# Optimization experiments

Hardware: AMD Instinct MI355X
Metric: run time of the kernel (lower is better)

The kernel has to match this reference:

```python
import jax, jax.numpy as jnp
import numpy as np

N_NODES = 100_000
N_EDGES = 1_600_000
F_IN = 32
F_OUT = 32
DIM = 2
K = 5                      # kernel_size per dim (open spline)
KTOT = K ** DIM            # 25 kernel weight matrices
S = 2 ** DIM               # 4 nonzero linear-B-spline basis terms per edge
NEG_SLOPE = 0.2

# offsets over the 2^DIM corners of the spline cell, [S, DIM]
_OFFSETS = np.array([[(s >> d) & 1 for d in range(DIM)] for s in range(S)], dtype=np.int32)
_STRIDES = np.array([K ** d for d in range(DIM)], dtype=np.int32)


def _spline_basis(pseudo):
    """Degree-1 open B-spline basis. pseudo: [E, DIM] in [0,1].
    Returns basis [E, S] and kernel-weight indices widx [E, S]."""
    offsets = jnp.asarray(_OFFSETS)
    strides = jnp.asarray(_STRIDES)
    p = pseudo * (K - 1)                         # open spline scaling
    fl = jnp.floor(p)
    frac = p - fl                                # [E, DIM]
    b = jnp.where(offsets[None] == 0, 1.0 - frac[:, None, :], frac[:, None, :])
    basis = jnp.prod(b, axis=-1)                 # [E, S]
    idx = jnp.clip(fl.astype(jnp.int32)[:, None, :] + offsets[None], 0, K - 1)
    widx = jnp.sum(idx * strides, axis=-1)       # [E, S] in [0, KTOT)
    return basis, widx


def setup_inputs() -> dict:
    key = jax.random.key(0)
    ks = jax.random.split(key, 7)
    x = jax.random.normal(ks[0], (N_NODES, F_IN), dtype=jnp.float32)
    edge_index = jax.random.randint(ks[1], (2, N_EDGES), 0, N_NODES)
    pseudo = jax.random.uniform(ks[2], (N_EDGES, DIM), dtype=jnp.float32)
    bound = 1.0 / np.sqrt(KTOT * F_IN)           # matches reset_parameters uniform(size, ...)
    weight = jax.random.uniform(ks[3], (KTOT, F_IN, F_OUT), jnp.float32, -bound, bound)
    root_weight = jax.random.uniform(ks[4], (F_IN, F_OUT), jnp.float32, -bound, bound)
    att_weight = jax.random.uniform(ks[5], (2 * F_OUT,), jnp.float32, -bound, bound)
    bias = jax.random.uniform(ks[6], (F_OUT,), jnp.float32, -bound, bound)
    return {"x": x, "edge_index": edge_index, "pseudo": pseudo, "weight": weight,
            "root_weight": root_weight, "att_weight": att_weight, "bias": bias}


def reference(x, edge_index, pseudo, weight, root_weight, att_weight, bias):
    row, col = edge_index[0], edge_index[1]      # row = target, col = source
    basis, widx = _spline_basis(pseudo)          # [E,S], [E,S]

    # Precompute x @ W_k for every kernel weight: [N, KTOT, F_OUT]
    xw = jnp.einsum('nf,kfo->nko', x, weight)
    flat = col[:, None] * KTOT + widx            # [E, S] flat (node, kernel) index
    gathered = xw.reshape(-1, F_OUT)[flat]       # [E, S, F_OUT]
    msg = jnp.einsum('es,esf->ef', basis, gathered)  # spline-weighted edge messages

    x_root = x @ root_weight                     # [N, F_OUT]

    # GAT-style attention logits: cat([x_root[row], msg]) . att_weight
    alpha = x_root[row] @ att_weight[:F_OUT] + msg @ att_weight[F_OUT:]
    alpha = jnp.where(alpha > 0, alpha, NEG_SLOPE * alpha)  # leaky relu

    # segment softmax over incoming edges of each target node
    amax = jax.ops.segment_max(alpha, row, num_segments=N_NODES)
    amax = jnp.where(jnp.isfinite(amax), amax, 0.0)
    ex = jnp.exp(alpha - amax[row])
    denom = jax.ops.segment_sum(ex, row, num_segments=N_NODES)
    att = ex / (denom[row] + 1e-16)

    out = jax.ops.segment_sum(msg * att[:, None], row, num_segments=N_NODES)
    return out + x_root + bias
```

## Files before the change

### kernel.cpp

```cpp
#include <hip/hip_runtime.h>
#include <stdint.h>

#define N_NODES 100000
#define N_EDGES 1600000
#define NBLK_SCAN 391

typedef __attribute__((ext_vector_type(8))) short short8;
typedef __attribute__((ext_vector_type(4))) float float4v;

__device__ __forceinline__ unsigned short f32_to_bf16(float f) {
  uint32_t u = __float_as_uint(f);
  u += 0x7fffu + ((u >> 16) & 1u);
  return (unsigned short)(u >> 16);
}
__device__ __forceinline__ float bf16_to_f32(unsigned short h) {
  return __uint_as_float(((uint32_t)h) << 16);
}

__global__ __launch_bounds__(256) void k_zero(
    const float* __restrict__ weight, const float* __restrict__ root_w,
    int* __restrict__ deg, unsigned short* __restrict__ wbf) {
  int tid = threadIdx.x;
  int b = blockIdx.x;
  int i = b * 256 + tid;
  if (i < N_NODES) deg[i] = 0;
  if (b < 100) {
    int e = i;
    int km = e >> 10;
    int rem = e & 1023;
    int kk = rem >> 5;
    int fo = rem & 31;
    int t = km * 2 + (fo >> 4);
    int c = fo & 15;
    int q = kk >> 3, j = kk & 7;
    wbf[((t * 4 + q) * 16 + c) * 8 + j] = f32_to_bf16(weight[e]);
  } else if (b == 100) {
    for (int idx = tid; idx < 1024; idx += 256) {
      int kk = idx >> 5;
      int fo = idx & 31;
      int t = 50 + (fo >> 4);
      int c = fo & 15;
      int q = kk >> 3, j = kk & 7;
      wbf[((t * 4 + q) * 16 + c) * 8 + j] = f32_to_bf16(root_w[idx]);
    }
  }
}

__global__ __launch_bounds__(256) void k1_xw(
    const float* __restrict__ x, const unsigned short* __restrict__ wbf,
    const int* __restrict__ ei, const float* __restrict__ att_w,
    const float* __restrict__ bias,
    int* __restrict__ deg, unsigned short* __restrict__ rank,
    unsigned short* __restrict__ xw, float* __restrict__ out,
    float* __restrict__ r_dot) {
  __shared__ __align__(16) unsigned short ot[16 * 808];
  __shared__ float xr[16][33];
  int tid = threadIdx.x;
  int b = blockIdx.x;

  int e = b * 256 + tid;
  int rk = atomicAdd(&deg[ei[e]], 1);

  int wave = tid >> 6, lane = tid & 63;
  int quad = lane >> 4, c16 = lane & 15;
  int n0 = b * 16;
  const float* xp = x + (size_t)(n0 + c16) * 32 + quad * 8;
  float4 a0 = *reinterpret_cast<const float4*>(xp);
  float4 a1 = *reinterpret_cast<const float4*>(xp + 4);
  short8 af;
  af[0] = (short)f32_to_bf16(a0.x); af[1] = (short)f32_to_bf16(a0.y);
  af[2] = (short)f32_to_bf16(a0.z); af[3] = (short)f32_to_bf16(a0.w);
  af[4] = (short)f32_to_bf16(a1.x); af[5] = (short)f32_to_bf16(a1.y);
  af[6] = (short)f32_to_bf16(a1.z); af[7] = (short)f32_to_bf16(a1.w);

  for (int t = wave; t < 52; t += 4) {
    short8 bf = *reinterpret_cast<const short8*>(wbf + ((t * 4 + quad) * 16 + c16) * 8);
    float4v acc = {0.f, 0.f, 0.f, 0.f};
    acc = __builtin_amdgcn_mfma_f32_16x16x32_bf16(af, bf, acc, 0, 0, 0);
    if (t < 50) {
      int cg = t * 16 + c16;
#pragma unroll
      for (int r = 0; r < 4; r++) ot[(quad * 4 + r) * 808 + cg] = f32_to_bf16(acc[r]);
    } else {
      int f = (t - 50) * 16 + c16;
#pragma unroll
      for (int r = 0; r < 4; r++) xr[quad * 4 + r][f] = acc[r];
    }
  }
  __syncthreads();

  const uint4* src = (const uint4*)ot;
  uint4* dst = (uint4*)(xw + (size_t)n0 * 800);
  for (int i = tid; i < 1600; i += 256) {
    int r = i / 100;
    int c = i - r * 100;
    dst[r * 100 + c] = src[r * 101 + c];
  }
  for (int idx = tid; idx < 512; idx += 256) {
    int n = idx >> 5, f = idx & 31;
    out[(n0 + n) * 32 + f] = xr[n][f] + bias[f];
  }
  if (tid < 16) {
    float s = 0.f;
#pragma unroll
    for (int f = 0; f < 32; f++) s += xr[tid][f] * att_w[f];
    r_dot[n0 + tid] = s;
  }
  rank[e] = (unsigned short)rk;
}

__global__ __launch_bounds__(256) void kscan1(const int* __restrict__ deg,
                                              int* __restrict__ incl,
                                              int* __restrict__ bsum) {
  __shared__ int s[256];
  int tid = threadIdx.x;
  int i = blockIdx.x * 256 + tid;
  int v = (i < N_NODES) ? deg[i] : 0;
  s[tid] = v;
  __syncthreads();
  for (int d = 1; d < 256; d <<= 1) {
    int t = (tid >= d) ? s[tid - d] : 0;
    __syncthreads();
    s[tid] += t;
    __syncthreads();
  }
  if (i < N_NODES) incl[i] = s[tid];
  if (tid == 255) bsum[blockIdx.x] = s[255];
}

__global__ __launch_bounds__(512) void kscan2(const int* __restrict__ bsum,
                                              int* __restrict__ bbase) {
  __shared__ int s[512];
  int tid = threadIdx.x;
  int v = (tid < NBLK_SCAN) ? bsum[tid] : 0;
  s[tid] = v;
  __syncthreads();
  for (int d = 1; d < 512; d <<= 1) {
    int t = (tid >= d) ? s[tid - d] : 0;
    __syncthreads();
    s[tid] += t;
    __syncthreads();
  }
  if (tid < NBLK_SCAN) bbase[tid] = s[tid] - v;
}

__global__ __launch_bounds__(256) void kscan3(const int* __restrict__ deg,
                                              int* __restrict__ offs,
                                              const int* __restrict__ bbase) {
  int i = blockIdx.x * 256 + threadIdx.x;
  if (i < N_NODES) offs[i] = offs[i] - deg[i] + bbase[i >> 8];
  if (i == 0) offs[N_NODES] = N_EDGES;
}

__global__ __launch_bounds__(256) void kscatter(
    const int* __restrict__ ei, const float* __restrict__ pseudo,
    const int* __restrict__ offs, const unsigned short* __restrict__ rank,
    uint2* __restrict__ epack) {
  int tid = threadIdx.x;
  int base = blockIdx.x * 2048;
#pragma unroll
  for (int k = 0; k < 8; k++) {
    int e = base + k * 256 + tid;
    if (e < N_EDGES) {
      int r = ei[e];
      int c = ei[N_EDGES + e];
      int pos = offs[r] + (int)rank[e];
      float p0 = pseudo[2 * e] * 4.f;
      float p1 = pseudo[2 * e + 1] * 4.f;
      float fl0 = floorf(p0), fl1 = floorf(p1);
      float fr0 = p0 - fl0, fr1 = p1 - fl1;
      int i0 = (int)fl0, i1 = (int)fl1;
      int a0 = min(i0, 4), a0p = min(i0 + 1, 4);
      int a1 = 5 * min(i1, 4), a1p = 5 * min(i1 + 1, 4);
      unsigned long long w0 = (unsigned long long)(a0 + a1);
      unsigned long long w1 = (unsigned long long)(a0p + a1);
      unsigned long long w2 = (unsigned long long)(a0 + a1p);
      unsigned long long w3 = (unsigned long long)(a0p + a1p);
      unsigned long long q0 = (unsigned long long)__float2uint_rn(fr0 * 8191.f);
      unsigned long long q1 = (unsigned long long)__float2uint_rn(fr1 * 8191.f);
      unsigned long long v = (unsigned long long)(unsigned int)c |
                             (w0 << 17) | (w1 << 22) | (w2 << 27) | (w3 << 32) |
                             (q0 << 37) | (q1 << 50);
      uint2 pk;
      pk.x = (unsigned int)v;
      pk.y = (unsigned int)(v >> 32);
      epack[pos] = pk;
    }
  }
}

__device__ __forceinline__ void decode_pk(uint2 pk, int& col, int& w0, int& w1,
                                          int& w2, int& w3, float& fr0, float& fr1) {
  unsigned long long v = ((unsigned long long)pk.y << 32) | pk.x;
  col = (int)(v & 0x1FFFF);
  w0 = (int)((v >> 17) & 31); w1 = (int)((v >> 22) & 31);
  w2 = (int)((v >> 27) & 31); w3 = (int)((v >> 32) & 31);
  fr0 = (float)(unsigned int)((v >> 37) & 8191) * (1.f / 8191.f);
  fr1 = (float)(unsigned int)((v >> 50) & 8191) * (1.f / 8191.f);
}

__device__ __forceinline__ void edge_step(uint2 pk, const unsigned short* __restrict__ xwf,
                                          float a2, float rd, float& acc, float& den) {
  int col, w0, w1, w2, w3; float fr0, fr1;
  decode_pk(pk, col, w0, w1, w2, w3, fr0, fr1);
  const unsigned short* base = xwf + (size_t)col * 800;
  float g0 = bf16_to_f32(base[w0 * 32]);
  float g1 = bf16_to_f32(base[w1 * 32]);
  float g2 = bf16_to_f32(base[w2 * 32]);
  float g3 = bf16_to_f32(base[w3 * 32]);
  float c0 = 1.f - fr0, c1 = 1.f - fr1;
  float msg = c1 * (c0 * g0 + fr0 * g1) + fr1 * (c0 * g2 + fr0 * g3);
  float t = msg * a2;
#pragma unroll
  for (int m = 16; m >= 1; m >>= 1) t += __shfl_xor(t, m);
  float alpha = rd + t;
  alpha = alpha > 0.f ? alpha : 0.2f * alpha;
  float ex = __expf(alpha);
  acc += msg * ex;
  den += ex;
}

__global__ __launch_bounds__(256) void k2_csr(
    const int* __restrict__ offs, const uint2* __restrict__ epack,
    const unsigned short* __restrict__ xw, const float* __restrict__ r_dot,
    const float* __restrict__ att_w, float* __restrict__ out) {
  int tid = threadIdx.x;
  int wave = tid >> 6, lane = tid & 63;
  int node = blockIdx.x * 4 + wave;
  if (node >= N_NODES) return;
  int f = lane & 31, half = lane >> 5;
  float a2 = att_w[32 + f];
  float rd = r_dot[node];
  int s0 = offs[node], s1 = offs[node + 1];
  const unsigned short* xwf = xw + f;
  float acc = 0.f, den = 0.f;
  int i = s0 + half;

  for (; i + 6 < s1; i += 8) {
    uint2 p[4];
    p[0] = epack[i];     p[1] = epack[i + 2];
    p[2] = epack[i + 4]; p[3] = epack[i + 6];
    int col[4], w0[4], w1[4], w2[4], w3[4];
    float fr0[4], fr1[4];
#pragma unroll
    for (int u = 0; u < 4; u++)
      decode_pk(p[u], col[u], w0[u], w1[u], w2[u], w3[u], fr0[u], fr1[u]);
    float g0[4], g1[4], g2[4], g3[4];
#pragma unroll
    for (int u = 0; u < 4; u++) {
      const unsigned short* base = xwf + (size_t)col[u] * 800;
      g0[u] = bf16_to_f32(base[w0[u] * 32]);
      g1[u] = bf16_to_f32(base[w1[u] * 32]);
      g2[u] = bf16_to_f32(base[w2[u] * 32]);
      g3[u] = bf16_to_f32(base[w3[u] * 32]);
    }
    float msg[4], t[4];
#pragma unroll
    for (int u = 0; u < 4; u++) {
      float c0 = 1.f - fr0[u], c1 = 1.f - fr1[u];
      msg[u] = c1 * (c0 * g0[u] + fr0[u] * g1[u]) + fr1[u] * (c0 * g2[u] + fr0[u] * g3[u]);
      t[u] = msg[u] * a2;
    }
#pragma unroll
    for (int m = 16; m >= 1; m >>= 1) {
      t[0] += __shfl_xor(t[0], m);
      t[1] += __shfl_xor(t[1], m);
      t[2] += __shfl_xor(t[2], m);
      t[3] += __shfl_xor(t[3], m);
    }
#pragma unroll
    for (int u = 0; u < 4; u++) {
      float alpha = rd + t[u];
      alpha = alpha > 0.f ? alpha : 0.2f * alpha;
      float ex = __expf(alpha);
      acc += msg[u] * ex;
      den += ex;
    }
  }
  for (; i < s1; i += 2) edge_step(epack[i], xwf, a2, rd, acc, den);

  acc += __shfl_xor(acc, 32);
  den += __shfl_xor(den, 32);
  if (half == 0) out[node * 32 + f] += acc / (den + 1e-16f);
}

extern "C" void kernel_launch(void* const* d_in, const int* in_sizes, int n_in,
                              void* d_out, int out_size, void* d_ws, size_t ws_size,
                              hipStream_t stream) {
  const float* x      = (const float*)d_in[0];
  const int*   ei     = (const int*)d_in[1];
  const float* pseudo = (const float*)d_in[2];
  const float* weight = (const float*)d_in[3];
  const float* root_w = (const float*)d_in[4];
  const float* att_w  = (const float*)d_in[5];
  const float* bias   = (const float*)d_in[6];
  float* out = (float*)d_out;

  char* ws = (char*)d_ws;
  unsigned short* xw   = (unsigned short*)ws;
  float* r_dot         = (float*)(ws + 160000000);
  unsigned short* wbf  = (unsigned short*)(ws + 160400000);
  int* deg             = (int*)(ws + 160453504);
  int* offs            = (int*)(ws + 160853504);
  int* bsum            = (int*)(ws + 161253520);
  int* bbase           = (int*)(ws + 161255120);
  unsigned short* rank = (unsigned short*)(ws + 161256720);
  uint2* epack         = (uint2*)(ws + 164456720);

  hipLaunchKernelGGL(k_zero, dim3(NBLK_SCAN), dim3(256), 0, stream,
                     weight, root_w, deg, wbf);
  hipLaunchKernelGGL(k1_xw, dim3(6250), dim3(256), 0, stream,
                     x, wbf, ei, att_w, bias, deg, rank, xw, out, r_dot);
  hipLaunchKernelGGL(kscan1, dim3(NBLK_SCAN), dim3(256), 0, stream, deg, offs, bsum);
  hipLaunchKernelGGL(kscan2, dim3(1), dim3(512), 0, stream, bsum, bbase);
  hipLaunchKernelGGL(kscan3, dim3(NBLK_SCAN), dim3(256), 0, stream, deg, offs, bbase);
  hipLaunchKernelGGL(kscatter, dim3(782), dim3(256), 0, stream,
                     ei, pseudo, offs, rank, epack);
  hipLaunchKernelGGL(k2_csr, dim3(25000), dim3(256), 0, stream,
                     offs, epack, xw, r_dot, att_w, out);
}
```

Baseline: 338.4 us.

## Precompute per-node kernel attention dots and fold softmax weights into per-edge coefficients

Adds a per-node, per-kernel table of the dot product between each xW_k row and the second half of the attention vector, computed in the xW kernel. The scatter kernel uses it to compute each edge's attention logit and exponential directly, and stores four bf16 basis-times-exp coefficients plus a compact index word per edge. The CSR aggregation kernel therefore drops its cross-lane shuffle reductions and exp work and reduces to a weighted gather-sum, using two accumulators. In exchange, the scatter kernel does extra random gathers into the new table, the softmax is computed without max subtraction, and the coefficients are rounded to bf16, so results may drift and large logits could overflow. Neighbouring spline weights are also addressed as w and w+1, which relies on a padding row that k_zero zeroes past the end of xw.

```diff
diff --git a/kernel.cpp b/kernel.cpp
--- a/kernel.cpp
+++ b/kernel.cpp
@@ -19,7 +19,8 @@
 
 __global__ __launch_bounds__(256) void k_zero(
     const float* __restrict__ weight, const float* __restrict__ root_w,
-    int* __restrict__ deg, unsigned short* __restrict__ wbf) {
+    int* __restrict__ deg, unsigned short* __restrict__ wbf,
+    unsigned short* __restrict__ xw, float* __restrict__ ydot) {
   int tid = threadIdx.x;
   int b = blockIdx.x;
   int i = b * 256 + tid;
@@ -39,10 +40,14 @@
       int kk = idx >> 5;
       int fo = idx & 31;
       int t = 50 + (fo >> 4);
-      int c = fo & 15;
+      int c = fo & 31 & 15;
       int q = kk >> 3, j = kk & 7;
-      wbf[((t * 4 + q) * 16 + c) * 8 + j] = f32_to_bf16(root_w[idx]);
-    }
+      wbf[((t * 4 + q) * 16 + (fo & 15)) * 8 + j] = f32_to_bf16(root_w[idx]);
+      (void)c;
+    }
+  } else if (b == 101) {
+    if (tid < 400) ((unsigned int*)(xw + 80000000))[tid] = 0u;
+    if (tid < 16) ydot[2500000 + tid] = 0.f;
   }
 }
 
@@ -52,11 +57,14 @@
     const float* __restrict__ bias,
     int* __restrict__ deg, unsigned short* __restrict__ rank,
     unsigned short* __restrict__ xw, float* __restrict__ out,
-    float* __restrict__ r_dot) {
+    float* __restrict__ r_dot, float* __restrict__ ydot) {
   __shared__ __align__(16) unsigned short ot[16 * 808];
   __shared__ float xr[16][33];
+  __shared__ float att2s[32];
   int tid = threadIdx.x;
   int b = blockIdx.x;
+
+  if (tid < 32) att2s[tid] = att_w[32 + tid];
 
   int e = b * 256 + tid;
   int rk = atomicAdd(&deg[ei[e]], 1);
@@ -100,6 +108,15 @@
     int n = idx >> 5, f = idx & 31;
     out[(n0 + n) * 32 + f] = xr[n][f] + bias[f];
   }
+  for (int idx = tid; idx < 400; idx += 256) {
+    int nd = idx / 25;
+    int km = idx - nd * 25;
+    const unsigned short* orow = ot + nd * 808 + km * 32;
+    float s = 0.f;
+#pragma unroll
+    for (int ff = 0; ff < 32; ff++) s += bf16_to_f32(orow[ff]) * att2s[ff];
+    ydot[(size_t)(n0 + nd) * 25 + km] = s;
+  }
   if (tid < 16) {
     float s = 0.f;
 #pragma unroll
@@ -155,7 +172,8 @@
 __global__ __launch_bounds__(256) void kscatter(
     const int* __restrict__ ei, const float* __restrict__ pseudo,
     const int* __restrict__ offs, const unsigned short* __restrict__ rank,
-    uint2* __restrict__ epack) {
+    const float* __restrict__ ydot, const float* __restrict__ r_dot,
+    unsigned int* __restrict__ eidx, uint2* __restrict__ ecoef) {
   int tid = threadIdx.x;
   int base = blockIdx.x * 2048;
 #pragma unroll
@@ -170,115 +188,93 @@
       float fl0 = floorf(p0), fl1 = floorf(p1);
       float fr0 = p0 - fl0, fr1 = p1 - fl1;
       int i0 = (int)fl0, i1 = (int)fl1;
-      int a0 = min(i0, 4), a0p = min(i0 + 1, 4);
-      int a1 = 5 * min(i1, 4), a1p = 5 * min(i1 + 1, 4);
-      unsigned long long w0 = (unsigned long long)(a0 + a1);
-      unsigned long long w1 = (unsigned long long)(a0p + a1);
-      unsigned long long w2 = (unsigned long long)(a0 + a1p);
-      unsigned long long w3 = (unsigned long long)(a0p + a1p);
-      unsigned long long q0 = (unsigned long long)__float2uint_rn(fr0 * 8191.f);
-      unsigned long long q1 = (unsigned long long)__float2uint_rn(fr1 * 8191.f);
-      unsigned long long v = (unsigned long long)(unsigned int)c |
-                             (w0 << 17) | (w1 << 22) | (w2 << 27) | (w3 << 32) |
-                             (q0 << 37) | (q1 << 50);
+      int w0 = min(i0, 4) + 5 * min(i1, 4);
+      int w2 = min(i0, 4) + 5 * min(i1 + 1, 4);
+      const float* yb = ydot + (size_t)c * 25;
+      float y0 = yb[w0], y1 = yb[w0 + 1];
+      float y2 = yb[w2], y3 = yb[w2 + 1];
+      float c0 = 1.f - fr0, c1 = 1.f - fr1;
+      float b0 = c0 * c1, b1 = fr0 * c1, b2 = c0 * fr1, b3 = fr0 * fr1;
+      float alpha = r_dot[r] + b0 * y0 + b1 * y1 + b2 * y2 + b3 * y3;
+      alpha = alpha > 0.f ? alpha : 0.2f * alpha;
+      float ex = __expf(alpha);
+      unsigned int q01 = (unsigned int)f32_to_bf16(b0 * ex) |
+                         ((unsigned int)f32_to_bf16(b1 * ex) << 16);
+      unsigned int q23 = (unsigned int)f32_to_bf16(b2 * ex) |
+                         ((unsigned int)f32_to_bf16(b3 * ex) << 16);
       uint2 pk;
-      pk.x = (unsigned int)v;
-      pk.y = (unsigned int)(v >> 32);
-      epack[pos] = pk;
-    }
-  }
-}
-
-__device__ __forceinline__ void decode_pk(uint2 pk, int& col, int& w0, int& w1,
-                                          int& w2, int& w3, float& fr0, float& fr1) {
-  unsigned long long v = ((unsigned long long)pk.y << 32) | pk.x;
-  col = (int)(v & 0x1FFFF);
-  w0 = (int)((v >> 17) & 31); w1 = (int)((v >> 22) & 31);
-  w2 = (int)((v >> 27) & 31); w3 = (int)((v >> 32) & 31);
-  fr0 = (float)(unsigned int)((v >> 37) & 8191) * (1.f / 8191.f);
-  fr1 = (float)(unsigned int)((v >> 50) & 8191) * (1.f / 8191.f);
-}
-
-__device__ __forceinline__ void edge_step(uint2 pk, const unsigned short* __restrict__ xwf,
-                                          float a2, float rd, float& acc, float& den) {
-  int col, w0, w1, w2, w3; float fr0, fr1;
-  decode_pk(pk, col, w0, w1, w2, w3, fr0, fr1);
-  const unsigned short* base = xwf + (size_t)col * 800;
-  float g0 = bf16_to_f32(base[w0 * 32]);
-  float g1 = bf16_to_f32(base[w1 * 32]);
-  float g2 = bf16_to_f32(base[w2 * 32]);
-  float g3 = bf16_to_f32(base[w3 * 32]);
-  float c0 = 1.f - fr0, c1 = 1.f - fr1;
-  float msg = c1 * (c0 * g0 + fr0 * g1) + fr1 * (c0 * g2 + fr0 * g3);
-  float t = msg * a2;
-#pragma unroll
-  for (int m = 16; m >= 1; m >>= 1) t += __shfl_xor(t, m);
-  float alpha = rd + t;
-  alpha = alpha > 0.f ? alpha : 0.2f * alpha;
-  float ex = __expf(alpha);
-  acc += msg * ex;
-  den += ex;
+      pk.x = q01;
+      pk.y = q23;
+      ecoef[pos] = pk;
+      eidx[pos] = (unsigned int)c | ((unsigned int)w0 << 17) |
+                  ((unsigned int)w2 << 22);
+    }
+  }
 }
 
 __global__ __launch_bounds__(256) void k2_csr(
-    const int* __restrict__ offs, const uint2* __restrict__ epack,
-    const unsigned short* __restrict__ xw, const float* __restrict__ r_dot,
-    const float* __restrict__ att_w, float* __restrict__ out) {
+    const int* __restrict__ offs, const unsigned int* __restrict__ eidx,
+    const uint2* __restrict__ ecoef, const unsigned short* __restrict__ xw,
+    float* __restrict__ out) {
   int tid = threadIdx.x;
   int wave = tid >> 6, lane = tid & 63;
   int node = blockIdx.x * 4 + wave;
   if (node >= N_NODES) return;
   int f = lane & 31, half = lane >> 5;
-  float a2 = att_w[32 + f];
-  float rd = r_dot[node];
   int s0 = offs[node], s1 = offs[node + 1];
   const unsigned short* xwf = xw + f;
-  float acc = 0.f, den = 0.f;
+  float accA = 0.f, accB = 0.f, denA = 0.f, denB = 0.f;
   int i = s0 + half;
 
   for (; i + 6 < s1; i += 8) {
-    uint2 p[4];
-    p[0] = epack[i];     p[1] = epack[i + 2];
-    p[2] = epack[i + 4]; p[3] = epack[i + 6];
-    int col[4], w0[4], w1[4], w2[4], w3[4];
-    float fr0[4], fr1[4];
-#pragma unroll
-    for (int u = 0; u < 4; u++)
-      decode_pk(p[u], col[u], w0[u], w1[u], w2[u], w3[u], fr0[u], fr1[u]);
+    unsigned int id[4];
+    uint2 cf[4];
+    id[0] = eidx[i];     id[1] = eidx[i + 2];
+    id[2] = eidx[i + 4]; id[3] = eidx[i + 6];
+    cf[0] = ecoef[i];     cf[1] = ecoef[i + 2];
+    cf[2] = ecoef[i + 4]; cf[3] = ecoef[i + 6];
     float g0[4], g1[4], g2[4], g3[4];
 #pragma unroll
     for (int u = 0; u < 4; u++) {
-      const unsigned short* base = xwf + (size_t)col[u] * 800;
-      g0[u] = bf16_to_f32(base[w0[u] * 32]);
-      g1[u] = bf16_to_f32(base[w1[u] * 32]);
-      g2[u] = bf16_to_f32(base[w2[u] * 32]);
-      g3[u] = bf16_to_f32(base[w3[u] * 32]);
-    }
-    float msg[4], t[4];
+      const unsigned short* base = xwf + (size_t)(id[u] & 0x1FFFF) * 800;
+      int o0 = ((id[u] >> 17) & 31) * 32;
+      int o2 = ((id[u] >> 22) & 31) * 32;
+      g0[u] = bf16_to_f32(base[o0]);
+      g1[u] = bf16_to_f32(base[o0 + 32]);
+      g2[u] = bf16_to_f32(base[o2]);
+      g3[u] = bf16_to_f32(base[o2 + 32]);
+    }
 #pragma unroll
     for (int u = 0; u < 4; u++) {
-      float c0 = 1.f - fr0[u], c1 = 1.f - fr1[u];
-      msg[u] = c1 * (c0 * g0[u] + fr0[u] * g1[u]) + fr1[u] * (c0 * g2[u] + fr0[u] * g3[u]);
-      t[u] = msg[u] * a2;
-    }
-#pragma unroll
-    for (int m = 16; m >= 1; m >>= 1) {
-      t[0] += __shfl_xor(t[0], m);
-      t[1] += __shfl_xor(t[1], m);
-      t[2] += __shfl_xor(t[2], m);
-      t[3] += __shfl_xor(t[3], m);
-    }
-#pragma unroll
-    for (int u = 0; u < 4; u++) {
-      float alpha = rd + t[u];
-      alpha = alpha > 0.f ? alpha : 0.2f * alpha;
-      float ex = __expf(alpha);
-      acc += msg[u] * ex;
-      den += ex;
-    }
-  }
-  for (; i < s1; i += 2) edge_step(epack[i], xwf, a2, rd, acc, den);
-
+      float q0 = __uint_as_float(cf[u].x << 16);
+      float q1 = __uint_as_float(cf[u].x & 0xffff0000u);
+      float q2 = __uint_as_float(cf[u].y << 16);
+      float q3 = __uint_as_float(cf[u].y & 0xffff0000u);
+      float m = q0 * g0[u] + q1 * g1[u] + q2 * g2[u] + q3 * g3[u];
+      float d = (q0 + q1) + (q2 + q3);
+      if (u & 1) { accB += m; denB += d; } else { accA += m; denA += d; }
+    }
+  }
+  for (; i < s1; i += 2) {
+    unsigned int idv = eidx[i];
+    uint2 cfv = ecoef[i];
+    const unsigned short* base = xwf + (size_t)(idv & 0x1FFFF) * 800;
+    int o0 = ((idv >> 17) & 31) * 32;
+    int o2 = ((idv >> 22) & 31) * 32;
+    float g0 = bf16_to_f32(base[o0]);
+    float g1 = bf16_to_f32(base[o0 + 32]);
+    float g2 = bf16_to_f32(base[o2]);
+    float g3 = bf16_to_f32(base[o2 + 32]);
+    float q0 = __uint_as_float(cfv.x << 16);
+    float q1 = __uint_as_float(cfv.x & 0xffff0000u);
+    float q2 = __uint_as_float(cfv.y << 16);
+    float q3 = __uint_as_float(cfv.y & 0xffff0000u);
+    accA += q0 * g0 + q1 * g1 + q2 * g2 + q3 * g3;
+    denA += (q0 + q1) + (q2 + q3);
+  }
+
+  float acc = accA + accB;
+  float den = denA + denB;
   acc += __shfl_xor(acc, 32);
   den += __shfl_xor(den, 32);
   if (half == 0) out[node * 32 + f] += acc / (den + 1e-16f);
@@ -298,24 +294,26 @@
 
   char* ws = (char*)d_ws;
   unsigned short* xw   = (unsigned short*)ws;
-  float* r_dot         = (float*)(ws + 160000000);
-  unsigned short* wbf  = (unsigned short*)(ws + 160400000);
-  int* deg             = (int*)(ws + 160453504);
-  int* offs            = (int*)(ws + 160853504);
-  int* bsum            = (int*)(ws + 161253520);
-  int* bbase           = (int*)(ws + 161255120);
-  unsigned short* rank = (unsigned short*)(ws + 161256720);
-  uint2* epack         = (uint2*)(ws + 164456720);
+  float* ydot          = (float*)(ws + 160001600);
+  float* r_dot         = (float*)(ws + 170001664);
+  unsigned short* wbf  = (unsigned short*)(ws + 170401664);
+  int* deg             = (int*)(ws + 170454912);
+  int* offs            = (int*)(ws + 170854912);
+  int* bsum            = (int*)(ws + 171254976);
+  int* bbase           = (int*)(ws + 171256576);
+  unsigned short* rank = (unsigned short*)(ws + 171258176);
+  uint2* ecoef         = (uint2*)(ws + 174458176);
+  unsigned int* eidx   = (unsigned int*)(ws + 187258176);
 
   hipLaunchKernelGGL(k_zero, dim3(NBLK_SCAN), dim3(256), 0, stream,
-                     weight, root_w, deg, wbf);
+                     weight, root_w, deg, wbf, xw, ydot);
   hipLaunchKernelGGL(k1_xw, dim3(6250), dim3(256), 0, stream,
-                     x, wbf, ei, att_w, bias, deg, rank, xw, out, r_dot);
+                     x, wbf, ei, att_w, bias, deg, rank, xw, out, r_dot, ydot);
   hipLaunchKernelGGL(kscan1, dim3(NBLK_SCAN), dim3(256), 0, stream, deg, offs, bsum);
   hipLaunchKernelGGL(kscan2, dim3(1), dim3(512), 0, stream, bsum, bbase);
   hipLaunchKernelGGL(kscan3, dim3(NBLK_SCAN), dim3(256), 0, stream, deg, offs, bbase);
   hipLaunchKernelGGL(kscatter, dim3(782), dim3(256), 0, stream,
-                     ei, pseudo, offs, rank, epack);
+                     ei, pseudo, offs, rank, ydot, r_dot, eidx, ecoef);
   hipLaunchKernelGGL(k2_csr, dim3(25000), dim3(256), 0, stream,
-                     offs, epack, xw, r_dot, att_w, out);
-}
+                     offs, eidx, ecoef, xw, out);
+}
```

New measurement: 400.5 us. 1.18x slower.
